# Optimization experiments

Hardware: AMD Instinct MI355X
Metric: run time of the kernel (lower is better)

## Reference

```python
import jax, jax.numpy as jnp
import numpy as np

N_EMBD = 1024
N_HEAD = 16
HEAD_DIM = N_EMBD // N_HEAD  # 64
R = 8
D_STD = HEAD_DIM - R         # 56
BLOCK_SIZE = 2048
B, T = 2, 2048
NEG = -1e9


def setup_inputs() -> dict:
    key = jax.random.key(0)
    ks = jax.random.split(key, 8)
    x = jax.random.normal(ks[0], (B, T, N_EMBD), dtype=jnp.float32)
    Wqkv = jax.random.normal(ks[1], (3 * N_EMBD, N_EMBD), dtype=jnp.float32) * 0.02
    Wproj = jax.random.normal(ks[2], (N_EMBD, N_EMBD), dtype=jnp.float32) * 0.02
    W_recip = jax.random.normal(ks[3], (HEAD_DIM, R), dtype=jnp.float32) * 0.02
    # mixing weights must be positive (sqrt is taken); match init scale
    w_std = jnp.full((N_HEAD,), 0.5, dtype=jnp.float32)
    w_rec = jnp.full((N_HEAD,), 0.3, dtype=jnp.float32)  # > threshold -> all heads RA
    w_disc = jnp.full((N_HEAD,), 0.2, dtype=jnp.float32)
    d_bias = jax.random.normal(ks[4], (N_HEAD, BLOCK_SIZE), dtype=jnp.float32) * 0.02
    return {"x": x, "Wqkv": Wqkv, "Wproj": Wproj, "W_recip": W_recip,
            "w_std": w_std, "w_rec": w_rec, "w_disc": w_disc, "d_bias": d_bias}


def reference(x, Wqkv, Wproj, W_recip, w_std, w_rec, w_disc, d_bias):
    Bx, Tx, C = x.shape
    H, hd = N_HEAD, HEAD_DIM
    qkv = x @ Wqkv.T                                   # (B,T,3C)
    q, k, v = jnp.split(qkv, 3, axis=-1)
    def heads(t):
        return t.reshape(Bx, Tx, H, hd).transpose(0, 2, 1, 3)  # (B,H,T,hd)
    q, k, v = heads(q), heads(k), heads(v)
    q_low = jnp.einsum('bhtd,dr->bhtr', q, W_recip)    # (B,H,T,R)
    k_low = jnp.einsum('bhtd,dr->bhtr', k, W_recip)
    sw_std = jnp.sqrt(w_std)[None, :, None, None]
    sw_rec = jnp.sqrt(w_rec)[None, :, None, None]
    # cross augmentation: q side carries k_low, k side carries q_low
    q_aug = jnp.concatenate([sw_std * q[..., :D_STD], sw_rec * k_low], axis=-1)
    k_aug = jnp.concatenate([sw_std * k[..., :D_STD], sw_rec * q_low], axis=-1)
    scale = 1.0 / jnp.sqrt(jnp.asarray(hd, dtype=x.dtype))
    scores = jnp.einsum('bhqd,bhkd->bhqk', q_aug, k_aug) * scale
    # per-head learned bias over key positions, broadcast over queries
    bias = w_disc[None, :, None, None] * d_bias[:, :Tx][None, :, None, :]
    scores = scores + bias
    causal = jnp.tril(jnp.ones((Tx, Tx), dtype=bool))
    scores = jnp.where(causal[None, None], scores, NEG)
    attn = jax.nn.softmax(scores, axis=-1)
    out = jnp.einsum('bhqk,bhkd->bhqd', attn, v)       # (B,H,T,hd)
    out = out.transpose(0, 2, 1, 3).reshape(Bx, Tx, C)
    return out @ Wproj.T
```

## Files before the change

kernel.cpp:

```cpp
#include <hip/hip_runtime.h>
#include <math.h>

#define T_SEQ 2048
#define NH 16
#define HD 64
#define CEMB 1024
#define NEGINF -3.0e38f
#define LOG2E 1.4426950408889634f

typedef unsigned short ushort;
typedef unsigned int uint;
typedef __attribute__((ext_vector_type(8))) short short8;
typedef __attribute__((ext_vector_type(4))) float f32x4;

#if __has_builtin(__builtin_amdgcn_exp2f)
#define EXP2(x) __builtin_amdgcn_exp2f(x)
#else
#define EXP2(x) exp2f(x)
#endif

__device__ __forceinline__ float b2f(ushort h) {
    union { uint u; float f; } cv; cv.u = ((uint)h) << 16; return cv.f;
}
__device__ __forceinline__ ushort f2b(float f) {
    union { float f; uint u; } cv; cv.f = f;
    return (ushort)((cv.u + 0x7FFF + ((cv.u >> 16) & 1)) >> 16);
}
__device__ __forceinline__ ushort f2b_fast(float f) {
    union { float f; uint u; } cv; cv.f = f;
    return (ushort)((cv.u + 0x8000) >> 16);
}
__device__ __forceinline__ uint pack_bf16(float a, float b) {
    union { float f; uint u; } ua, ub; ua.f = a; ub.f = b;
    return __builtin_amdgcn_perm(ub.u + 0x8000u, ua.u + 0x8000u, 0x07060302u);
}
__device__ __forceinline__ void gl2lds16(const ushort* g, ushort* l) {
    __builtin_amdgcn_global_load_lds(
        (const __attribute__((address_space(1))) void*)g,
        (__attribute__((address_space(3))) void*)l, 16, 0, 0);
}

__global__ __launch_bounds__(256) void convert_all_kernel(
    const float* __restrict__ x, const float* __restrict__ wqkv,
    const float* __restrict__ wproj,
    ushort* __restrict__ xb, ushort* __restrict__ wqkvb,
    ushort* __restrict__ wprojb)
{
    const int bid = blockIdx.x;
    const float* src; ushort* dst; int off;
    if (bid < 4096)      { src = x;     dst = xb;     off = bid; }
    else if (bid < 7168) { src = wqkv;  dst = wqkvb;  off = bid - 4096; }
    else                 { src = wproj; dst = wprojb; off = bid - 7168; }
    const int i = (off * 256 + threadIdx.x) * 4;
    const float4 v = *(const float4*)&src[i];
    ushort4 o;
    o.x = f2b(v.x); o.y = f2b(v.y); o.z = f2b(v.z); o.w = f2b(v.w);
    *(ushort4*)&dst[i] = o;
}

__global__ __launch_bounds__(256) void wlow_kernel(
    const float* __restrict__ Wqkv, const float* __restrict__ W_recip,
    const float* __restrict__ w_disc, const float* __restrict__ d_bias,
    ushort* __restrict__ wqkvb, float* __restrict__ bias_pre)
{
    const int bid = blockIdx.x;
    if (bid >= 32) {
        const int h = bid - 32;
        const float wd = w_disc[h] * LOG2E;
        const int j = h * T_SEQ + threadIdx.x * 8;
        const float4 a = *(const float4*)&d_bias[j];
        const float4 c = *(const float4*)&d_bias[j + 4];
        float4 oa, oc;
        oa.x = a.x * wd; oa.y = a.y * wd; oa.z = a.z * wd; oa.w = a.w * wd;
        oc.x = c.x * wd; oc.y = c.y * wd; oc.z = c.z * wd; oc.w = c.w * wd;
        *(float4*)&bias_pre[j] = oa;
        *(float4*)&bias_pre[j + 4] = oc;
        return;
    }
    const int qk = bid >> 4, h = bid & 15;
    const int e0 = threadIdx.x * 4;
    f32x4 acc[8];
    #pragma unroll
    for (int r = 0; r < 8; ++r) acc[r] = (f32x4){0.f, 0.f, 0.f, 0.f};
    for (int d = 0; d < 64; ++d) {
        const float4 xv = *(const float4*)&Wqkv[(size_t)(qk * 1024 + h * 64 + d) * 1024 + e0];
        #pragma unroll
        for (int r = 0; r < 8; ++r) {
            const float w = W_recip[d * 8 + r];
            acc[r][0] = fmaf(w, xv.x, acc[r][0]);
            acc[r][1] = fmaf(w, xv.y, acc[r][1]);
            acc[r][2] = fmaf(w, xv.z, acc[r][2]);
            acc[r][3] = fmaf(w, xv.w, acc[r][3]);
        }
    }
    #pragma unroll
    for (int r = 0; r < 8; ++r) {
        ushort4 o;
        o.x = f2b(acc[r][0]); o.y = f2b(acc[r][1]);
        o.z = f2b(acc[r][2]); o.w = f2b(acc[r][3]);
        *(ushort4*)&wqkvb[(size_t)(3072 + qk * 128 + h * 8 + r) * 1024 + e0] = o;
    }
}

#define GEMM_CORE(Aptr, Bptr, KDIM, SMEMN)                                     \
    __shared__ __align__(16) ushort SMEM[SMEMN];                               \
    ushort* const Asl = SMEM;                                                  \
    ushort* const Bsl = SMEM + 4096;                                           \
    const int row0 = blockIdx.x * 128;                                         \
    const int col0 = blockIdx.y * 128;                                         \
    const int tid = threadIdx.x;                                               \
    const int wave = tid >> 6, lane = tid & 63;                                \
    const int wm = wave >> 1, wn = wave & 1;                                   \
    const int quad = lane >> 4, lq = lane & 15;                                \
    f32x4 acc[4][4];                                                           \
    _Pragma("unroll") for (int i = 0; i < 4; ++i)                              \
        _Pragma("unroll") for (int j = 0; j < 4; ++j)                          \
            acc[i][j] = (f32x4){0.f, 0.f, 0.f, 0.f};                           \
    for (int k0 = 0; k0 < (KDIM); k0 += 32) {                                  \
        _Pragma("unroll") for (int r2 = 0; r2 < 2; ++r2) {                     \
            const int c = r2 * 256 + tid;                                      \
            const int row = c >> 2, kc = (c & 3) * 8;                          \
            gl2lds16(&(Aptr)[(size_t)(row0 + row) * (KDIM) + k0 + kc], &Asl[c * 8]); \
            gl2lds16(&(Bptr)[(size_t)(col0 + row) * (KDIM) + k0 + kc], &Bsl[c * 8]); \
        }                                                                      \
        __syncthreads();                                                       \
        short8 af[4], bf[4];                                                   \
        _Pragma("unroll") for (int i = 0; i < 4; ++i)                          \
            af[i] = *(const short8*)&Asl[(wm * 64 + i * 16 + lq) * 32 + quad * 8]; \
        _Pragma("unroll") for (int j = 0; j < 4; ++j)                          \
            bf[j] = *(const short8*)&Bsl[(wn * 64 + j * 16 + lq) * 32 + quad * 8]; \
        _Pragma("unroll") for (int i = 0; i < 4; ++i)                          \
            _Pragma("unroll") for (int j = 0; j < 4; ++j)                      \
                acc[i][j] = __builtin_amdgcn_mfma_f32_16x16x32_bf16(           \
                    af[i], bf[j], acc[i][j], 0, 0, 0);                         \
        __syncthreads();                                                       \
    }

__global__ __launch_bounds__(256, 4) void gemm_qkv_kernel(
    const ushort* __restrict__ A, const ushort* __restrict__ Bt,
    const float* __restrict__ w_std, const float* __restrict__ w_rec,
    ushort* __restrict__ qh, ushort* __restrict__ kh, ushort* __restrict__ vt)
{
    GEMM_CORE(A, Bt, 1024, 128 * 136)
    ushort* const Cs = SMEM;

    if (col0 >= 2048 && col0 < 3072) {
        #pragma unroll
        for (int j = 0; j < 4; ++j) {
            const int cc = col0 + wn * 64 + j * 16 + lq;
            const int h = (cc >> 6) & 15;
            const int d = cc & 63;
            #pragma unroll
            for (int i = 0; i < 4; ++i) {
                const int rr0 = row0 + wm * 64 + i * 16 + quad * 4;
                const int b = rr0 >> 11, t0 = rr0 & 2047;
                ushort4 pv;
                pv.x = f2b(acc[i][j][0]); pv.y = f2b(acc[i][j][1]);
                pv.z = f2b(acc[i][j][2]); pv.w = f2b(acc[i][j][3]);
                *(ushort4*)&vt[((((size_t)b * NH + h) * HD + d) * T_SEQ + t0)] = pv;
            }
        }
    } else if (col0 < 2048) {
        const bool isq = (col0 < 1024);
        #pragma unroll
        for (int j = 0; j < 4; ++j) {
            const int colc = wn * 64 + j * 16 + lq;
            const int h = ((col0 + colc) >> 6) & 15;
            const float sc = isq ? w_std[h] * (0.125f * LOG2E) : 1.0f;
            #pragma unroll
            for (int i = 0; i < 4; ++i)
                #pragma unroll
                for (int r = 0; r < 4; ++r)
                    Cs[(wm * 64 + i * 16 + quad * 4 + r) * 136 + colc] =
                        f2b(acc[i][j][r] * sc);
        }
        __syncthreads();
        ushort* dst = isq ? qh : kh;
        const int hbase = (col0 >> 6) & 15;
        #pragma unroll
        for (int rep = 0; rep < 8; ++rep) {
            const int id = rep * 256 + tid;
            const int row = id >> 4, chunk = id & 15;
            if ((chunk & 7) == 7) continue;
            const int h = hbase + (chunk >> 3);
            const int d = (chunk & 7) * 8;
            const int rr = row0 + row;
            const int b = rr >> 11, t = rr & 2047;
            const uint4 val = *(const uint4*)&Cs[row * 136 + chunk * 8];
            *(uint4*)&dst[((((size_t)b * NH + h) * T_SEQ + t) * HD + d)] = val;
        }
    } else {
        const bool isqlow = (col0 < 3200);
        #pragma unroll
        for (int j = 0; j < 4; ++j) {
            const int colc = wn * 64 + j * 16 + lq;
            const int h = colc >> 3;
            const float sc = isqlow ? 1.0f : w_rec[h] * (0.125f * LOG2E);
            #pragma unroll
            for (int i = 0; i < 4; ++i)
                #pragma unroll
                for (int r = 0; r < 4; ++r)
                    Cs[(wm * 64 + i * 16 + quad * 4 + r) * 136 + colc] =
                        f2b(acc[i][j][r] * sc);
        }
        __syncthreads();
        ushort* dst = isqlow ? kh : qh;
        #pragma unroll
        for (int rep = 0; rep < 8; ++rep) {
            const int id = rep * 256 + tid;
            const int row = id >> 4, h = id & 15;
            const int rr = row0 + row;
            const int b = rr >> 11, t = rr & 2047;
            const uint4 val = *(const uint4*)&Cs[row * 136 + h * 8];
            *(uint4*)&dst[((((size_t)b * NH + h) * T_SEQ + t) * HD + 56)] = val;
        }
    }
}

__global__ __launch_bounds__(256) void gemm_proj_kernel(
    const ushort* __restrict__ A, const ushort* __restrict__ Bt,
    float* __restrict__ C)
{
    GEMM_CORE(A, Bt, 1024, 8192)
    #pragma unroll
    for (int i = 0; i < 4; ++i) {
        #pragma unroll
        for (int r = 0; r < 4; ++r) {
            const int rr = row0 + wm * 64 + i * 16 + quad * 4 + r;
            #pragma unroll
            for (int j = 0; j < 4; ++j) {
                const int cc = col0 + wn * 64 + j * 16 + lq;
                C[(size_t)rr * 1024 + cc] = acc[i][j][r];
            }
        }
    }
}

__global__ __launch_bounds__(256, 4) void attn_kernel(
    const ushort* __restrict__ qa, const ushort* __restrict__ ka,
    const ushort* __restrict__ vt, const float* __restrict__ bias_pre,
    ushort* __restrict__ out)
{
    __shared__ __align__(16) ushort Qs[64 * 64];
    __shared__ __align__(16) ushort KPs[128 * 64];
    __shared__ __align__(16) ushort Vs[64 * 128];
    const int bh = blockIdx.x;
    const int qt = 31 - blockIdx.y;
    const int h = bh & 15;
    const int b = bh >> 4;
    const int tid = threadIdx.x;
    const int wave = tid >> 6, lane = tid & 63;
    const int quad = lane >> 4, lq = lane & 15;
    const int l7 = lq & 7;
    const size_t base = (size_t)bh * T_SEQ * HD;

    #pragma unroll
    for (int rep = 0; rep < 2; ++rep) {
        const int idx = rep * 256 + tid;
        const int row = idx >> 3, slot = idx & 7;
        gl2lds16(&qa[base + (size_t)(qt * 64 + row) * 64 + ((slot ^ (row & 7)) << 3)],
                 &Qs[idx * 8]);
    }
    __syncthreads();
    short8 bq[2];
    #pragma unroll
    for (int ks = 0; ks < 2; ++ks)
        bq[ks] = *(const short8*)&Qs[(wave * 16 + lq) * 64 + (((ks * 4 + quad) ^ l7) << 3)];

    f32x4 o4[4];
    #pragma unroll
    for (int dt = 0; dt < 4; ++dt) o4[dt] = (f32x4){0.f, 0.f, 0.f, 0.f};
    float lsum = 0.f;
    const int qrow = qt * 64 + wave * 16 + lq;
    const int prow = (wave * 16 + lq) * 128;
    const int nchunks = (qt + 2) >> 1;
    const float* bias_h = &bias_pre[h * T_SEQ];

    for (int c = 0; c < nchunks; ++c) {
        const int k0 = c * 128;
        if (c) __syncthreads();
        #pragma unroll
        for (int rep = 0; rep < 4; ++rep) {
            const int idx = rep * 256 + tid;
            const int row = idx >> 3, slot = idx & 7;
            gl2lds16(&ka[base + (size_t)(k0 + row) * 64 + ((slot ^ (row & 7)) << 3)],
                     &KPs[idx * 8]);
        }
        #pragma unroll
        for (int rep = 0; rep < 4; ++rep) {
            const int idx = rep * 256 + tid;
            const int row = idx >> 4, slot = idx & 15;
            gl2lds16(&vt[base + (size_t)row * T_SEQ + k0 + ((slot ^ (row & 15)) << 3)],
                     &Vs[idx * 8]);
        }
        __syncthreads();

        f32x4 s4[8];
        #pragma unroll
        for (int nt = 0; nt < 8; ++nt)
            s4[nt] = *(const f32x4*)&bias_h[k0 + nt * 16 + quad * 4];
        #pragma unroll
        for (int ks = 0; ks < 2; ++ks)
            #pragma unroll
            for (int nt = 0; nt < 8; ++nt) {
                const short8 ak = *(const short8*)
                    &KPs[(nt * 16 + lq) * 64 + (((ks * 4 + quad) ^ l7) << 3)];
                s4[nt] = __builtin_amdgcn_mfma_f32_16x16x32_bf16(
                    ak, bq[ks], s4[nt], 0, 0, 0);
            }
        __syncthreads();

        const bool lastc = (c == nchunks - 1);
        #pragma unroll
        for (int nt = 0; nt < 8; ++nt) {
            f32x4 sv = s4[nt];
            if (lastc) {
                const int kb = k0 + nt * 16 + quad * 4;
                #pragma unroll
                for (int r = 0; r < 4; ++r)
                    if (kb + r > qrow) sv[r] = NEGINF;
            }
            const float p0 = EXP2(sv[0]), p1 = EXP2(sv[1]);
            const float p2 = EXP2(sv[2]), p3 = EXP2(sv[3]);
            lsum += (p0 + p1) + (p2 + p3);
            const int pcol = (nt * 16 + quad * 4) ^ (l7 << 3);
            uint2 pv; pv.x = pack_bf16(p0, p1); pv.y = pack_bf16(p2, p3);
            *(uint2*)&KPs[prow + pcol] = pv;
        }

        #pragma unroll
        for (int ks = 0; ks < 4; ++ks) {
            const short8 bp = *(const short8*)
                &KPs[prow + ((ks * 32 + quad * 8) ^ (l7 << 3))];
            #pragma unroll
            for (int dt = 0; dt < 4; ++dt) {
                const short8 av = *(const short8*)
                    &Vs[(dt * 16 + lq) * 128 + (((ks * 4 + quad) ^ lq) << 3)];
                o4[dt] = __builtin_amdgcn_mfma_f32_16x16x32_bf16(
                    av, bp, o4[dt], 0, 0, 0);
            }
        }
    }

    lsum += __shfl_xor(lsum, 16, 64);
    lsum += __shfl_xor(lsum, 32, 64);
    const float inv = 1.0f / lsum;
    const size_t obase = ((size_t)b * T_SEQ + qrow) * CEMB + h * HD;
    #pragma unroll
    for (int dt = 0; dt < 4; ++dt) {
        ushort4 ov;
        ov.x = f2b_fast(o4[dt][0] * inv);
        ov.y = f2b_fast(o4[dt][1] * inv);
        ov.z = f2b_fast(o4[dt][2] * inv);
        ov.w = f2b_fast(o4[dt][3] * inv);
        *(ushort4*)&out[obase + dt * 16 + quad * 4] = ov;
    }
}

extern "C" void kernel_launch(void* const* d_in, const int* in_sizes, int n_in,
                              void* d_out, int out_size, void* d_ws, size_t ws_size,
                              hipStream_t stream) {
    const float* x       = (const float*)d_in[0];
    const float* Wqkv    = (const float*)d_in[1];
    const float* Wproj   = (const float*)d_in[2];
    const float* W_recip = (const float*)d_in[3];
    const float* w_std   = (const float*)d_in[4];
    const float* w_rec   = (const float*)d_in[5];
    const float* w_disc  = (const float*)d_in[6];
    const float* d_bias  = (const float*)d_in[7];
    float* out = (float*)d_out;

    const size_t NX = (size_t)4096 * 1024;
    const size_t NWQKVX = (size_t)3328 * 1024;
    const size_t NWPROJ = (size_t)1024 * 1024;
    ushort* xb     = (ushort*)d_ws;
    ushort* wqkvb  = xb + NX;
    ushort* wprojb = wqkvb + NWQKVX;
    ushort* qh     = wprojb + NWPROJ;
    ushort* kh     = qh + NX;
    ushort* vt     = kh + NX;
    ushort* ao     = vt + NX;
    float*  bias_pre = (float*)(ao + NX);

    convert_all_kernel<<<8192, 256, 0, stream>>>(x, Wqkv, Wproj, xb, wqkvb, wprojb);
    wlow_kernel<<<48, 256, 0, stream>>>(Wqkv, W_recip, w_disc, d_bias, wqkvb, bias_pre);
    gemm_qkv_kernel<<<dim3(32, 26), 256, 0, stream>>>(xb, wqkvb, w_std, w_rec, qh, kh, vt);
    attn_kernel<<<dim3(32, 32), 256, 0, stream>>>(qh, kh, vt, bias_pre, ao);
    gemm_proj_kernel<<<dim3(32, 8), 256, 0, stream>>>(ao, wprojb, out);
}
```

Measured before the change: 210.8 us.

## Merge prep kernels and deepen GEMM K-tile with XOR-swizzled LDS layout

Merges the fp32-to-bf16 conversion kernel and the low-rank weight/bias kernel into a single launch to cut one kernel launch. The shared GEMM core now stages 64-wide K tiles instead of 32, halving the number of barrier pairs per K loop, and XOR-swizzles the 16-byte LDS slots by row to avoid bank conflicts on fragment reads. This doubles LDS use for the projection GEMM, which also gets a launch-bounds occupancy hint. The gemm_qkv SMEM of 128*136 still fits the larger B offset.

```diff
diff --git a/kernel.cpp b/kernel.cpp
--- a/kernel.cpp
+++ b/kernel.cpp
@@ -40,32 +40,28 @@
         (__attribute__((address_space(3))) void*)l, 16, 0, 0);
 }
 
-__global__ __launch_bounds__(256) void convert_all_kernel(
-    const float* __restrict__ x, const float* __restrict__ wqkv,
-    const float* __restrict__ wproj,
+__global__ __launch_bounds__(256) void prep_kernel(
+    const float* __restrict__ x, const float* __restrict__ Wqkv,
+    const float* __restrict__ Wproj, const float* __restrict__ W_recip,
+    const float* __restrict__ w_disc, const float* __restrict__ d_bias,
     ushort* __restrict__ xb, ushort* __restrict__ wqkvb,
-    ushort* __restrict__ wprojb)
+    ushort* __restrict__ wprojb, float* __restrict__ bias_pre)
 {
     const int bid = blockIdx.x;
-    const float* src; ushort* dst; int off;
-    if (bid < 4096)      { src = x;     dst = xb;     off = bid; }
-    else if (bid < 7168) { src = wqkv;  dst = wqkvb;  off = bid - 4096; }
-    else                 { src = wproj; dst = wprojb; off = bid - 7168; }
-    const int i = (off * 256 + threadIdx.x) * 4;
-    const float4 v = *(const float4*)&src[i];
-    ushort4 o;
-    o.x = f2b(v.x); o.y = f2b(v.y); o.z = f2b(v.z); o.w = f2b(v.w);
-    *(ushort4*)&dst[i] = o;
-}
-
-__global__ __launch_bounds__(256) void wlow_kernel(
-    const float* __restrict__ Wqkv, const float* __restrict__ W_recip,
-    const float* __restrict__ w_disc, const float* __restrict__ d_bias,
-    ushort* __restrict__ wqkvb, float* __restrict__ bias_pre)
-{
-    const int bid = blockIdx.x;
-    if (bid >= 32) {
-        const int h = bid - 32;
+    if (bid < 8192) {
+        const float* src; ushort* dst; int off;
+        if (bid < 4096)      { src = x;     dst = xb;     off = bid; }
+        else if (bid < 7168) { src = Wqkv;  dst = wqkvb;  off = bid - 4096; }
+        else                 { src = Wproj; dst = wprojb; off = bid - 7168; }
+        const int i = (off * 256 + threadIdx.x) * 4;
+        const float4 v = *(const float4*)&src[i];
+        ushort4 o;
+        o.x = f2b(v.x); o.y = f2b(v.y); o.z = f2b(v.z); o.w = f2b(v.w);
+        *(ushort4*)&dst[i] = o;
+        return;
+    }
+    if (bid >= 8224) {
+        const int h = bid - 8224;
         const float wd = w_disc[h] * LOG2E;
         const int j = h * T_SEQ + threadIdx.x * 8;
         const float4 a = *(const float4*)&d_bias[j];
@@ -77,11 +73,13 @@
         *(float4*)&bias_pre[j + 4] = oc;
         return;
     }
-    const int qk = bid >> 4, h = bid & 15;
+    const int wb = bid - 8192;
+    const int qk = wb >> 4, h = wb & 15;
     const int e0 = threadIdx.x * 4;
     f32x4 acc[8];
     #pragma unroll
     for (int r = 0; r < 8; ++r) acc[r] = (f32x4){0.f, 0.f, 0.f, 0.f};
+    #pragma unroll 4
     for (int d = 0; d < 64; ++d) {
         const float4 xv = *(const float4*)&Wqkv[(size_t)(qk * 1024 + h * 64 + d) * 1024 + e0];
         #pragma unroll
@@ -105,34 +103,40 @@
 #define GEMM_CORE(Aptr, Bptr, KDIM, SMEMN)                                     \
     __shared__ __align__(16) ushort SMEM[SMEMN];                               \
     ushort* const Asl = SMEM;                                                  \
-    ushort* const Bsl = SMEM + 4096;                                           \
+    ushort* const Bsl = SMEM + 8192;                                           \
     const int row0 = blockIdx.x * 128;                                         \
     const int col0 = blockIdx.y * 128;                                         \
     const int tid = threadIdx.x;                                               \
     const int wave = tid >> 6, lane = tid & 63;                                \
     const int wm = wave >> 1, wn = wave & 1;                                   \
     const int quad = lane >> 4, lq = lane & 15;                                \
+    const int l7 = lq & 7;                                                     \
     f32x4 acc[4][4];                                                           \
     _Pragma("unroll") for (int i = 0; i < 4; ++i)                              \
         _Pragma("unroll") for (int j = 0; j < 4; ++j)                          \
             acc[i][j] = (f32x4){0.f, 0.f, 0.f, 0.f};                           \
-    for (int k0 = 0; k0 < (KDIM); k0 += 32) {                                  \
-        _Pragma("unroll") for (int r2 = 0; r2 < 2; ++r2) {                     \
-            const int c = r2 * 256 + tid;                                      \
-            const int row = c >> 2, kc = (c & 3) * 8;                          \
-            gl2lds16(&(Aptr)[(size_t)(row0 + row) * (KDIM) + k0 + kc], &Asl[c * 8]); \
-            gl2lds16(&(Bptr)[(size_t)(col0 + row) * (KDIM) + k0 + kc], &Bsl[c * 8]); \
+    for (int k0 = 0; k0 < (KDIM); k0 += 64) {                                  \
+        _Pragma("unroll") for (int p = 0; p < 4; ++p) {                        \
+            const int idx = p * 256 + tid;                                     \
+            const int row = idx >> 3, slot = idx & 7;                          \
+            const int kc = (slot ^ (row & 7)) << 3;                            \
+            gl2lds16(&(Aptr)[(size_t)(row0 + row) * (KDIM) + k0 + kc], &Asl[idx * 8]); \
+            gl2lds16(&(Bptr)[(size_t)(col0 + row) * (KDIM) + k0 + kc], &Bsl[idx * 8]); \
         }                                                                      \
         __syncthreads();                                                       \
-        short8 af[4], bf[4];                                                   \
-        _Pragma("unroll") for (int i = 0; i < 4; ++i)                          \
-            af[i] = *(const short8*)&Asl[(wm * 64 + i * 16 + lq) * 32 + quad * 8]; \
-        _Pragma("unroll") for (int j = 0; j < 4; ++j)                          \
-            bf[j] = *(const short8*)&Bsl[(wn * 64 + j * 16 + lq) * 32 + quad * 8]; \
-        _Pragma("unroll") for (int i = 0; i < 4; ++i)                          \
+        _Pragma("unroll") for (int ks = 0; ks < 2; ++ks) {                     \
+            short8 af[4], bf[4];                                               \
+            _Pragma("unroll") for (int i = 0; i < 4; ++i)                      \
+                af[i] = *(const short8*)&Asl[(wm * 64 + i * 16 + lq) * 64 +    \
+                                             (((ks * 4 + quad) ^ l7) << 3)];   \
             _Pragma("unroll") for (int j = 0; j < 4; ++j)                      \
-                acc[i][j] = __builtin_amdgcn_mfma_f32_16x16x32_bf16(           \
-                    af[i], bf[j], acc[i][j], 0, 0, 0);                         \
+                bf[j] = *(const short8*)&Bsl[(wn * 64 + j * 16 + lq) * 64 +    \
+                                             (((ks * 4 + quad) ^ l7) << 3)];   \
+            _Pragma("unroll") for (int i = 0; i < 4; ++i)                      \
+                _Pragma("unroll") for (int j = 0; j < 4; ++j)                  \
+                    acc[i][j] = __builtin_amdgcn_mfma_f32_16x16x32_bf16(       \
+                        af[i], bf[j], acc[i][j], 0, 0, 0);                     \
+        }                                                                      \
         __syncthreads();                                                       \
     }
 
@@ -217,11 +221,11 @@
     }
 }
 
-__global__ __launch_bounds__(256) void gemm_proj_kernel(
+__global__ __launch_bounds__(256, 4) void gemm_proj_kernel(
     const ushort* __restrict__ A, const ushort* __restrict__ Bt,
     float* __restrict__ C)
 {
-    GEMM_CORE(A, Bt, 1024, 8192)
+    GEMM_CORE(A, Bt, 1024, 16384)
     #pragma unroll
     for (int i = 0; i < 4; ++i) {
         #pragma unroll
@@ -382,8 +386,8 @@
     ushort* ao     = vt + NX;
     float*  bias_pre = (float*)(ao + NX);
 
-    convert_all_kernel<<<8192, 256, 0, stream>>>(x, Wqkv, Wproj, xb, wqkvb, wprojb);
-    wlow_kernel<<<48, 256, 0, stream>>>(Wqkv, W_recip, w_disc, d_bias, wqkvb, bias_pre);
+    prep_kernel<<<8240, 256, 0, stream>>>(x, Wqkv, Wproj, W_recip, w_disc, d_bias,
+                                          xb, wqkvb, wprojb, bias_pre);
     gemm_qkv_kernel<<<dim3(32, 26), 256, 0, stream>>>(xb, wqkvb, w_std, w_rec, qh, kh, vt);
     attn_kernel<<<dim3(32, 32), 256, 0, stream>>>(qh, kh, vt, bias_pre, ao);
     gemm_proj_kernel<<<dim3(32, 8), 256, 0, stream>>>(ao, wprojb, out);
```

Result: faster. 191.8 us (-9.0%).
